# Kernel tuning notes

Measured on AMD Instinct MI355X. Metric: run time of the kernel, lower is better.

Reference implementation:

```python
import jax, jax.numpy as jnp
import numpy as np

D_MODEL = 1024
EXPAND = 2
D_INNER = D_MODEL * EXPAND
KERNEL = 4
EPS = 1e-5


def setup_inputs() -> dict:
    key = jax.random.key(0)
    ks = jax.random.split(key, 8)
    B, L = 2, 4096
    x = jax.random.normal(ks[0], (B, L, D_MODEL), dtype=jnp.float32)
    norm_w = jnp.ones((D_MODEL,), jnp.float32)
    norm_b = jnp.zeros((D_MODEL,), jnp.float32)
    # torch Linear weight layout [out, in]
    in_proj_w = jax.random.normal(ks[1], (2 * D_INNER, D_MODEL), jnp.float32) / np.sqrt(D_MODEL)
    # depthwise Conv1d weight [d_inner, 1, K]
    conv_w = jax.random.normal(ks[2], (D_INNER, 1, KERNEL), jnp.float32) / np.sqrt(KERNEL)
    conv_b = jax.random.normal(ks[3], (D_INNER,), jnp.float32) * 0.02
    gate_w = jax.random.normal(ks[4], (D_INNER, D_INNER), jnp.float32) / np.sqrt(D_INNER)
    gate_b = jnp.zeros((D_INNER,), jnp.float32)
    out_proj_w = jax.random.normal(ks[5], (D_MODEL, D_INNER), jnp.float32) / np.sqrt(D_INNER)
    return {"x": x, "norm_w": norm_w, "norm_b": norm_b, "in_proj_w": in_proj_w,
            "conv_w": conv_w, "conv_b": conv_b, "gate_w": gate_w, "gate_b": gate_b,
            "out_proj_w": out_proj_w}


def _layernorm(x, w, b):
    mu = jnp.mean(x, axis=-1, keepdims=True)
    var = jnp.var(x, axis=-1, keepdims=True)
    return (x - mu) * jax.lax.rsqrt(var + EPS) * w + b


def _glru(x, norm_w, norm_b, in_proj_w, conv_w, conv_b, gate_w, gate_b, out_proj_w):
    B, L, D = x.shape
    residual = x
    xn = _layernorm(x, norm_w, norm_b)
    xz = jnp.einsum('bld,ed->ble', xn, in_proj_w)  # [B,L,2*d_inner]
    x_inner, z = jnp.split(xz, 2, axis=-1)
    # causal depthwise conv: torch pads 3 both sides then slices [:L] == left-pad 3
    lhs = jnp.transpose(x_inner, (0, 2, 1))  # [B, C, L]
    conv = jax.lax.conv_general_dilated(
        lhs, conv_w, window_strides=(1,), padding=[(KERNEL - 1, 0)],
        feature_group_count=D_INNER,
        dimension_numbers=('NCH', 'OIH', 'NCH'))
    x_conv = jnp.transpose(conv, (0, 2, 1)) + conv_b  # [B, L, C]
    x_conv = jax.nn.silu(x_conv)
    a = jax.nn.sigmoid(jnp.einsum('blc,ec->ble', x_conv, gate_w) + gate_b)
    b = (1.0 - a) * x_conv
    # h_t = a_t * h_{t-1} + b_t, h_0 prior = 0 -> parallel associative scan
    def combine(e1, e2):
        a1, b1 = e1
        a2, b2 = e2
        return a1 * a2, a2 * b1 + b2
    _, y = jax.lax.associative_scan(combine, (a, b), axis=1)
    y = y * jax.nn.silu(z)
    return residual + jnp.einsum('blc,dc->bld', y, out_proj_w)


def reference(x, norm_w, norm_b, in_proj_w, conv_w, conv_b, gate_w, gate_b, out_proj_w):
    return _glru(x, norm_w, norm_b, in_proj_w, conv_w, conv_b, gate_w, gate_b, out_proj_w)
```

## Files before the change

kernel.cpp:

```cpp
#include <hip/hip_runtime.h>
#include <cstdint>

#define D_MODEL 1024
#define D_INNER 2048
#define LSEQ    4096
#define BATCH   2
#define M_ROWS  (BATCH * LSEQ)
#define CHUNK   128
#define NCHUNK  (LSEQ / CHUNK)

typedef unsigned short u16;
typedef __bf16 bf16x8 __attribute__((ext_vector_type(8)));
typedef float f32x4 __attribute__((ext_vector_type(4)));
typedef u16 u16x4 __attribute__((ext_vector_type(4)));

__device__ __forceinline__ u16 f2bf(float f) {
  union { float f; unsigned u; } x; x.f = f;
  unsigned u = x.u;
  unsigned r = (u + 0x7FFFu + ((u >> 16) & 1u)) >> 16;
  return (u16)r;
}
__device__ __forceinline__ float bf2f(u16 h) {
  union { unsigned u; float f; } x; x.u = ((unsigned)h) << 16;
  return x.f;
}
__device__ __forceinline__ float sigmoidf_(float v) { return 1.0f / (1.0f + expf(-v)); }
__device__ __forceinline__ float siluf_(float v)    { return v / (1.0f + expf(-v)); }

__device__ __forceinline__ void gl_lds16(const void* g, void* l) {
  __builtin_amdgcn_global_load_lds(
      (const __attribute__((address_space(1))) void*)g,
      (__attribute__((address_space(3))) void*)l, 16, 0, 0);
}

#define SBAR()   asm volatile("s_barrier" ::: "memory")
#define WAITV0() asm volatile("s_waitcnt vmcnt(0)" ::: "memory")
#define WAITV4() asm volatile("s_waitcnt vmcnt(4)" ::: "memory")

__global__ void __launch_bounds__(256)
cast_bf16_kernel(const float* __restrict__ in, u16* __restrict__ out, int n4) {
  int i = blockIdx.x * 256 + threadIdx.x;
  if (i < n4) {
    float4 v = ((const float4*)in)[i];
    u16x4 o;
    o.x = f2bf(v.x); o.y = f2bf(v.y); o.z = f2bf(v.z); o.w = f2bf(v.w);
    ((u16x4*)out)[i] = o;
  }
}

__global__ void __launch_bounds__(256)
ln_kernel(const float* __restrict__ x, const float* __restrict__ w,
          const float* __restrict__ b, u16* __restrict__ xn) {
  const int row = blockIdx.x;
  const int t = threadIdx.x;
  const float4 v = ((const float4*)(x + (size_t)row * D_MODEL))[t];
  float s  = v.x + v.y + v.z + v.w;
  float ss = v.x * v.x + v.y * v.y + v.z * v.z + v.w * v.w;
#pragma unroll
  for (int o = 32; o > 0; o >>= 1) {
    s  += __shfl_xor(s, o);
    ss += __shfl_xor(ss, o);
  }
  __shared__ float red[8];
  const int wid = t >> 6, lane = t & 63;
  if (lane == 0) { red[wid] = s; red[4 + wid] = ss; }
  __syncthreads();
  s  = red[0] + red[1] + red[2] + red[3];
  ss = red[4] + red[5] + red[6] + red[7];
  const float mu  = s * (1.0f / D_MODEL);
  const float var = ss * (1.0f / D_MODEL) - mu * mu;
  const float rs  = rsqrtf(var + 1e-5f);
  const float4 wv = ((const float4*)w)[t];
  const float4 bv = ((const float4*)b)[t];
  u16x4 o4;
  o4.x = f2bf((v.x - mu) * rs * wv.x + bv.x);
  o4.y = f2bf((v.y - mu) * rs * wv.y + bv.y);
  o4.z = f2bf((v.z - mu) * rs * wv.z + bv.z);
  o4.w = f2bf((v.w - mu) * rs * wv.w + bv.w);
  ((u16x4*)(xn + (size_t)row * D_MODEL))[t] = o4;
}

#define MFMA_BF16 __builtin_amdgcn_mfma_f32_16x16x32_bf16

template<int EPI>
__global__ void __launch_bounds__(256, 2)
gemm128(const u16* __restrict__ A, const u16* __restrict__ Bm,
        int M, int N, int K,
        const float* __restrict__ ef, float* __restrict__ of,
        u16* __restrict__ ob0, u16* __restrict__ ob1) {
  __shared__ __align__(1024) char lds[65536];
  const int tid  = threadIdx.x;
  const int wid  = tid >> 6, lane = tid & 63;
  const int nbx  = N >> 7;
  const int nwg  = nbx * (M >> 7);
  const int bid  = blockIdx.x;
  const int cpx  = nwg >> 3;
  const int swzb = (bid & 7) * cpx + (bid >> 3);
  const int bx   = swzb % nbx, by = swzb / nbx;
  const size_t m0 = (size_t)by << 7, n0 = (size_t)bx << 7;
  const int wr = wid >> 1, wc = wid & 1;
  const size_t rb = (size_t)K * 2;

  const int sslot = (((lane & 3) ^ ((lane >> 3) & 3)) << 4);
  const char* gA = (const char*)A  + (m0 + (size_t)(wid * 16 + (lane >> 2))) * rb + sslot;
  const char* gB = (const char*)Bm + (n0 + (size_t)(wid * 16 + (lane >> 2))) * rb + sslot;
  const int sd = wid * 1024;

  const int q = lane >> 4, r15 = lane & 15;
  const int xr = ((q ^ ((r15 >> 1) & 3)) << 4);
  const int aoff = (wr * 64 + r15) * 64 + xr;
  const int boff = (wc * 64 + r15) * 64 + xr;

  f32x4 acc[4][4] = {};
  const int nk = K >> 6;

  auto STG = [&](const char* g, char* ldsbase, int kk, int r0, size_t kbv) {
    gl_lds16(g + kbv + kk * 64 + (size_t)r0 * rb, ldsbase + kk * 8192 + r0 * 64 + sd);
  };

  STG(gA, lds, 0, 0, 0); STG(gA, lds, 0, 64, 0);
  STG(gB, lds + 16384, 0, 0, 0); STG(gB, lds + 16384, 0, 64, 0);
  STG(gA, lds, 1, 0, 0); STG(gA, lds, 1, 64, 0);
  STG(gB, lds + 16384, 1, 0, 0); STG(gB, lds + 16384, 1, 64, 0);
  WAITV4();
  SBAR();

  size_t kb = 128;
  for (int t = 0; t < nk; ++t) {
    const int cur = t & 1;
    const char* Ac = lds + cur * 32768;
    const char* Bc = Ac + 16384;
    char* An = lds + ((cur ^ 1) * 32768);
    char* Bn = An + 16384;
    const bool pf = (t + 1 < nk);
    bf16x8 af[4], bf[4];

    if (pf) {
      STG(gA, An, 0, 0, kb); STG(gA, An, 0, 64, kb);
      STG(gB, Bn, 0, 0, kb); STG(gB, Bn, 0, 64, kb);
    }
#pragma unroll
    for (int mi = 0; mi < 4; ++mi) af[mi] = *(const bf16x8*)(Ac + aoff + mi * 1024);
#pragma unroll
    for (int ni = 0; ni < 4; ++ni) bf[ni] = *(const bf16x8*)(Bc + boff + ni * 1024);
    __builtin_amdgcn_s_setprio(1);
#pragma unroll
    for (int mi = 0; mi < 4; ++mi)
#pragma unroll
      for (int ni = 0; ni < 4; ++ni)
        acc[mi][ni] = MFMA_BF16(af[mi], bf[ni], acc[mi][ni], 0, 0, 0);
    __builtin_amdgcn_s_setprio(0);
    if (pf) { WAITV4(); } else { WAITV0(); }
    SBAR();

    if (pf) {
      STG(gA, An, 1, 0, kb); STG(gA, An, 1, 64, kb);
      STG(gB, Bn, 1, 0, kb); STG(gB, Bn, 1, 64, kb);
    }
#pragma unroll
    for (int mi = 0; mi < 4; ++mi) af[mi] = *(const bf16x8*)(Ac + 8192 + aoff + mi * 1024);
#pragma unroll
    for (int ni = 0; ni < 4; ++ni) bf[ni] = *(const bf16x8*)(Bc + 8192 + boff + ni * 1024);
    __builtin_amdgcn_s_setprio(1);
#pragma unroll
    for (int mi = 0; mi < 4; ++mi)
#pragma unroll
      for (int ni = 0; ni < 4; ++ni)
        acc[mi][ni] = MFMA_BF16(af[mi], bf[ni], acc[mi][ni], 0, 0, 0);
    __builtin_amdgcn_s_setprio(0);
    if (pf) { WAITV4(); SBAR(); }
    kb += 128;
  }

  const int c0 = lane & 15;
  const int r0 = (lane >> 4) << 2;
  const bool isz = (EPI == 0) && (n0 >= (size_t)D_INNER);
#pragma unroll
  for (int mi = 0; mi < 4; ++mi) {
#pragma unroll
    for (int ni = 0; ni < 4; ++ni) {
#pragma unroll
      for (int rg = 0; rg < 4; ++rg) {
        const size_t row = m0 + (size_t)(wr * 64 + mi * 16 + r0 + rg);
        const size_t col = n0 + (size_t)(wc * 64 + ni * 16 + c0);
        const float v = acc[mi][ni][rg];
        if (EPI == 0) {
          if (!isz) ob0[row * D_INNER + col] = f2bf(v);
          else      ob1[row * D_INNER + (col - D_INNER)] = f2bf(siluf_(v));
        } else if (EPI == 1) {
          ob0[row * (size_t)N + col] = f2bf(v);
        } else {
          of[row * (size_t)N + col] = v + ef[row * (size_t)N + col];
        }
      }
    }
  }
}

__global__ void __launch_bounds__(256)
conv_silu_kernel(const u16* __restrict__ xin, const float* __restrict__ cw,
                 const float* __restrict__ cb, u16* __restrict__ xc) {
  const int c   = blockIdx.x * 256 + threadIdx.x;
  const int l0  = blockIdx.y * 8;
  const int bat = blockIdx.z;
  const size_t base = ((size_t)bat * LSEQ) * D_INNER + c;
  const float w0 = cw[c * 4 + 0], w1 = cw[c * 4 + 1], w2 = cw[c * 4 + 2], w3 = cw[c * 4 + 3];
  const float bb = cb[c];
  float v[11];
#pragma unroll
  for (int i = 0; i < 11; ++i) {
    const int l = l0 - 3 + i;
    v[i] = (l >= 0) ? bf2f(xin[base + (size_t)l * D_INNER]) : 0.0f;
  }
#pragma unroll
  for (int r = 0; r < 8; ++r) {
    const float acc = bb + w0 * v[r] + w1 * v[r + 1] + w2 * v[r + 2] + w3 * v[r + 3];
    xc[base + (size_t)(l0 + r) * D_INNER] = f2bf(siluf_(acc));
  }
}

__global__ void __launch_bounds__(256)
scan_a_kernel(const u16* __restrict__ g, const u16* __restrict__ xc,
              const float* __restrict__ gbias,
              float* __restrict__ cA, float* __restrict__ cB) {
  const int c   = (blockIdx.x * 256 + threadIdx.x) * 2;
  const int ch  = blockIdx.y;
  const int bat = blockIdx.z;
  const float bb0 = gbias[c], bb1 = gbias[c + 1];
  size_t idx = ((size_t)bat * LSEQ + (size_t)ch * CHUNK) * D_INNER + c;
  float pA0 = 1.0f, hB0 = 0.0f, pA1 = 1.0f, hB1 = 0.0f;
  for (int t = 0; t < CHUNK; ++t) {
    const ushort2 gg = *(const ushort2*)(g + idx);
    const ushort2 xx = *(const ushort2*)(xc + idx);
    const float a0 = sigmoidf_(bf2f(gg.x) + bb0);
    const float a1 = sigmoidf_(bf2f(gg.y) + bb1);
    pA0 *= a0; hB0 = a0 * hB0 + (1.0f - a0) * bf2f(xx.x);
    pA1 *= a1; hB1 = a1 * hB1 + (1.0f - a1) * bf2f(xx.y);
    idx += D_INNER;
  }
  const size_t o = ((size_t)bat * NCHUNK + ch) * D_INNER + c;
  *(float2*)(cA + o) = make_float2(pA0, pA1);
  *(float2*)(cB + o) = make_float2(hB0, hB1);
}

__global__ void __launch_bounds__(256)
scan_b_kernel(const float* __restrict__ cA, const float* __restrict__ cB,
              float* __restrict__ carry) {
  const int tid = blockIdx.x * 256 + threadIdx.x;
  const int bat = tid >> 11;
  const int c   = tid & (D_INNER - 1);
  float h = 0.0f;
  const size_t base = (size_t)bat * NCHUNK * D_INNER + c;
  for (int i = 0; i < NCHUNK; ++i) {
    const size_t o = base + (size_t)i * D_INNER;
    carry[o] = h;
    h = cA[o] * h + cB[o];
  }
}

__global__ void __launch_bounds__(256)
scan_c_kernel(const u16* __restrict__ g, const u16* __restrict__ xc,
              const u16* __restrict__ sz, const float* __restrict__ gbias,
              const float* __restrict__ carry, u16* __restrict__ yg) {
  const int c   = (blockIdx.x * 256 + threadIdx.x) * 2;
  const int ch  = blockIdx.y;
  const int bat = blockIdx.z;
  const float bb0 = gbias[c], bb1 = gbias[c + 1];
  const float2 h2 = *(const float2*)(carry + ((size_t)bat * NCHUNK + ch) * D_INNER + c);
  float h0 = h2.x, h1 = h2.y;
  size_t idx = ((size_t)bat * LSEQ + (size_t)ch * CHUNK) * D_INNER + c;
  for (int t = 0; t < CHUNK; ++t) {
    const ushort2 gg = *(const ushort2*)(g + idx);
    const ushort2 xx = *(const ushort2*)(xc + idx);
    const ushort2 zz = *(const ushort2*)(sz + idx);
    const float a0 = sigmoidf_(bf2f(gg.x) + bb0);
    const float a1 = sigmoidf_(bf2f(gg.y) + bb1);
    h0 = a0 * h0 + (1.0f - a0) * bf2f(xx.x);
    h1 = a1 * h1 + (1.0f - a1) * bf2f(xx.y);
    ushort2 o2;
    o2.x = f2bf(h0 * bf2f(zz.x));
    o2.y = f2bf(h1 * bf2f(zz.y));
    *(ushort2*)(yg + idx) = o2;
    idx += D_INNER;
  }
}

extern "C" void kernel_launch(void* const* d_in, const int* in_sizes, int n_in,
                              void* d_out, int out_size, void* d_ws, size_t ws_size,
                              hipStream_t stream) {
  const float* x         = (const float*)d_in[0];
  const float* norm_w    = (const float*)d_in[1];
  const float* norm_b    = (const float*)d_in[2];
  const float* in_proj_w = (const float*)d_in[3];
  const float* conv_w    = (const float*)d_in[4];
  const float* conv_b    = (const float*)d_in[5];
  const float* gate_w    = (const float*)d_in[6];
  const float* gate_b    = (const float*)d_in[7];
  const float* out_proj_w= (const float*)d_in[8];
  float* out = (float*)d_out;

  char* p = (char*)d_ws;
  u16* xn      = (u16*)p; p += (size_t)M_ROWS * D_MODEL * 2;
  u16* w_in    = (u16*)p; p += (size_t)2 * D_INNER * D_MODEL * 2;
  u16* w_gate  = (u16*)p; p += (size_t)D_INNER * D_INNER * 2;
  u16* w_out   = (u16*)p; p += (size_t)D_MODEL * D_INNER * 2;
  u16* x_inner = (u16*)p; p += (size_t)M_ROWS * D_INNER * 2;
  u16* szb     = (u16*)p; p += (size_t)M_ROWS * D_INNER * 2;
  u16* xconv   = (u16*)p; p += (size_t)M_ROWS * D_INNER * 2;
  u16* gbuf    = (u16*)p; p += (size_t)M_ROWS * D_INNER * 2;
  u16* yg      = (u16*)p; p += (size_t)M_ROWS * D_INNER * 2;
  float* cA    = (float*)p; p += (size_t)BATCH * NCHUNK * D_INNER * 4;
  float* cB    = (float*)p; p += (size_t)BATCH * NCHUNK * D_INNER * 4;
  float* carry = (float*)p; p += (size_t)BATCH * NCHUNK * D_INNER * 4;
  if ((size_t)(p - (char*)d_ws) > ws_size) return;

  cast_bf16_kernel<<<dim3(2 * D_INNER * D_MODEL / 4 / 256), 256, 0, stream>>>(in_proj_w, w_in, 2 * D_INNER * D_MODEL / 4);
  cast_bf16_kernel<<<dim3(D_INNER * D_INNER / 4 / 256), 256, 0, stream>>>(gate_w, w_gate, D_INNER * D_INNER / 4);
  cast_bf16_kernel<<<dim3(D_MODEL * D_INNER / 4 / 256), 256, 0, stream>>>(out_proj_w, w_out, D_MODEL * D_INNER / 4);

  ln_kernel<<<dim3(M_ROWS), 256, 0, stream>>>(x, norm_w, norm_b, xn);

  gemm128<0><<<dim3((M_ROWS / 128) * (2 * D_INNER / 128)), 256, 0, stream>>>(
      xn, w_in, M_ROWS, 2 * D_INNER, D_MODEL, nullptr, nullptr, x_inner, szb);

  conv_silu_kernel<<<dim3(D_INNER / 256, LSEQ / 8, BATCH), 256, 0, stream>>>(x_inner, conv_w, conv_b, xconv);

  gemm128<1><<<dim3((M_ROWS / 128) * (D_INNER / 128)), 256, 0, stream>>>(
      xconv, w_gate, M_ROWS, D_INNER, D_INNER, nullptr, nullptr, gbuf, nullptr);

  scan_a_kernel<<<dim3(D_INNER / 512, NCHUNK, BATCH), 256, 0, stream>>>(gbuf, xconv, gate_b, cA, cB);
  scan_b_kernel<<<dim3(BATCH * D_INNER / 256), 256, 0, stream>>>(cA, cB, carry);
  scan_c_kernel<<<dim3(D_INNER / 512, NCHUNK, BATCH), 256, 0, stream>>>(gbuf, xconv, szb, gate_b, carry, yg);

  gemm128<2><<<dim3((M_ROWS / 128) * (D_MODEL / 128)), 256, 0, stream>>>(
      yg, w_out, M_ROWS, D_MODEL, D_INNER, x, out, nullptr, nullptr);
}
```

Baseline: 362.9 us.

## Add 256x256 8-wave ping-pong GEMM for in_proj and gate projections

Adds a new GEMM kernel with 512 threads and 256x256 output tiles. It uses 128 KB of LDS, double-buffered with 128-wide K steps, and interleaves global-to-LDS staging with MFMA phases separated by barriers. Each wave now covers 128x64, which raises arithmetic intensity per LDS byte and cuts global traffic per FLOP. The in_proj and gate GEMMs use it; the out_proj GEMM stays on the old 128x128 kernel. In exchange there is one block per CU, fewer workgroups (256 and 128), and many barriers per iteration.

```diff
diff --git a/kernel.cpp b/kernel.cpp
--- a/kernel.cpp
+++ b/kernel.cpp
@@ -36,6 +36,7 @@
 #define SBAR()   asm volatile("s_barrier" ::: "memory")
 #define WAITV0() asm volatile("s_waitcnt vmcnt(0)" ::: "memory")
 #define WAITV4() asm volatile("s_waitcnt vmcnt(4)" ::: "memory")
+#define WAITL0() do { asm volatile("s_waitcnt lgkmcnt(0)" ::: "memory"); __builtin_amdgcn_sched_barrier(0); } while (0)
 
 __global__ void __launch_bounds__(256)
 cast_bf16_kernel(const float* __restrict__ in, u16* __restrict__ out, int n4) {
@@ -81,6 +82,157 @@
 }
 
 #define MFMA_BF16 __builtin_amdgcn_mfma_f32_16x16x32_bf16
+
+template<int EPI>
+__global__ void __launch_bounds__(512, 1)
+gemm8p(const u16* __restrict__ A, const u16* __restrict__ Bm,
+       int M, int N, int K,
+       const float* __restrict__ ef, float* __restrict__ of,
+       u16* __restrict__ ob0, u16* __restrict__ ob1) {
+  __shared__ __align__(1024) char lds[131072];
+  const int tid  = threadIdx.x;
+  const int wid  = tid >> 6, lane = tid & 63;
+  const int nbx  = N >> 8;
+  const int nwg  = nbx * (M >> 8);
+  const int bid  = blockIdx.x;
+  const int cpx  = nwg >> 3;
+  const int swzb = (bid & 7) * cpx + (bid >> 3);
+  const int bx   = swzb % nbx, by = swzb / nbx;
+  const size_t m0 = (size_t)by << 8, n0 = (size_t)bx << 8;
+  const int wr = wid >> 2, wc = wid & 3;
+  const size_t rb = (size_t)K * 2;
+
+  const int strow = lane >> 3;
+  const int stchk = (lane & 7) ^ strow;
+  const char* gA = (const char*)A  + (m0 + (size_t)(wid * 8 + strow)) * rb + stchk * 16;
+  const char* gB = (const char*)Bm + (n0 + (size_t)(wid * 8 + strow)) * rb + stchk * 16;
+  const int sdw = wid * 1024;
+
+  auto ST_A = [&](int t, int h) {
+    char* d = lds + (t & 1) * 32768 + h * 16384 + sdw;
+    const char* s = gA + (size_t)t * 128 + (size_t)(h * 128) * rb;
+    gl_lds16(s, d);
+    gl_lds16(s + 64 * rb, d + 8192);
+  };
+  auto ST_B = [&](int t, int h) {
+    char* d = lds + 65536 + (t & 1) * 32768 + h * 16384 + sdw;
+    const char* s = gB + (size_t)t * 128 + (size_t)(h * 128) * rb;
+    gl_lds16(s, d);
+    gl_lds16(s + 64 * rb, d + 8192);
+  };
+
+  const int q = lane >> 4, r15 = lane & 15;
+  const int kx0 = ((q ^ (r15 & 7)) << 4);
+  const int kx1 = (((4 + q) ^ (r15 & 7)) << 4);
+  const int arow = r15 * 128;
+  const int brow = ((wc & 1) * 64 + r15) * 128;
+  const char* aE = lds + wr * 16384;
+  const char* bE = lds + 65536 + (wc >> 1) * 16384;
+  const char* aO = aE + 32768;
+  const char* bO = bE + 32768;
+
+  bf16x8 af[8], bf[4];
+  f32x4 acc[8][4] = {};
+
+#define RD_A(kx, base)  _Pragma("unroll") \
+    for (int mf = 0; mf < 8; ++mf) af[mf] = *(const bf16x8*)((base) + mf * 2048 + arow + (kx));
+#define RD_B(kx, base)  _Pragma("unroll") \
+    for (int nf = 0; nf < 4; ++nf) bf[nf] = *(const bf16x8*)((base) + nf * 2048 + brow + (kx));
+#define MM_LO() do { __builtin_amdgcn_s_setprio(1); _Pragma("unroll") \
+    for (int mf = 0; mf < 8; ++mf) { \
+      acc[mf][0] = MFMA_BF16(af[mf], bf[0], acc[mf][0], 0, 0, 0); \
+      acc[mf][1] = MFMA_BF16(af[mf], bf[1], acc[mf][1], 0, 0, 0); } \
+    __builtin_amdgcn_s_setprio(0); } while (0)
+#define MM_HI() do { __builtin_amdgcn_s_setprio(1); _Pragma("unroll") \
+    for (int mf = 0; mf < 8; ++mf) { \
+      acc[mf][2] = MFMA_BF16(af[mf], bf[2], acc[mf][2], 0, 0, 0); \
+      acc[mf][3] = MFMA_BF16(af[mf], bf[3], acc[mf][3], 0, 0, 0); } \
+    __builtin_amdgcn_s_setprio(0); } while (0)
+
+  const int nk = K >> 6;
+  const int nIter = nk >> 1;
+
+  ST_A(0, 0); ST_A(0, 1); ST_B(0, 0); ST_B(0, 1);
+  ST_A(1, 0); ST_A(1, 1);
+  WAITV4();
+  SBAR();
+
+  for (int i = 0; i < nIter; ++i) {
+    const int t1 = 2 * i + 1, t2 = 2 * i + 2, t3 = 2 * i + 3;
+    const bool pf = (t2 < nk);
+
+    RD_A(kx0, aE); RD_B(kx0, bE);
+    ST_B(t1, 0);
+    SBAR(); WAITL0();
+    MM_LO();
+    SBAR();
+
+    ST_B(t1, 1);
+    SBAR();
+    MM_HI();
+    SBAR();
+
+    RD_A(kx1, aE); RD_B(kx1, bE);
+    SBAR(); WAITL0();
+    MM_LO();
+    SBAR();
+
+    if (pf) { ST_A(t2, 0); ST_A(t2, 1); WAITV4(); } else { WAITV0(); }
+    SBAR();
+    MM_HI();
+    SBAR();
+
+    RD_A(kx0, aO); RD_B(kx0, bO);
+    if (pf) ST_B(t2, 0);
+    SBAR(); WAITL0();
+    MM_LO();
+    SBAR();
+
+    if (pf) ST_B(t2, 1);
+    SBAR();
+    MM_HI();
+    SBAR();
+
+    RD_A(kx1, aO); RD_B(kx1, bO);
+    SBAR(); WAITL0();
+    MM_LO();
+    SBAR();
+
+    if (pf) { ST_A(t3, 0); ST_A(t3, 1); WAITV4(); }
+    SBAR();
+    MM_HI();
+    SBAR();
+  }
+
+#undef RD_A
+#undef RD_B
+#undef MM_LO
+#undef MM_HI
+
+  const int c0 = lane & 15;
+  const int r0 = (lane >> 4) << 2;
+  const bool isz = (EPI == 0) && (n0 >= (size_t)D_INNER);
+#pragma unroll
+  for (int mf = 0; mf < 8; ++mf) {
+#pragma unroll
+    for (int nf = 0; nf < 4; ++nf) {
+#pragma unroll
+      for (int rg = 0; rg < 4; ++rg) {
+        const size_t row = m0 + (size_t)(wr * 128 + mf * 16 + r0 + rg);
+        const size_t col = n0 + (size_t)(wc * 64 + nf * 16 + c0);
+        const float v = acc[mf][nf][rg];
+        if (EPI == 0) {
+          if (!isz) ob0[row * D_INNER + col] = f2bf(v);
+          else      ob1[row * D_INNER + (col - D_INNER)] = f2bf(siluf_(v));
+        } else if (EPI == 1) {
+          ob0[row * (size_t)N + col] = f2bf(v);
+        } else {
+          of[row * (size_t)N + col] = v + ef[row * (size_t)N + col];
+        }
+      }
+    }
+  }
+}
 
 template<int EPI>
 __global__ void __launch_bounds__(256, 2)
@@ -114,8 +266,8 @@
   f32x4 acc[4][4] = {};
   const int nk = K >> 6;
 
-  auto STG = [&](const char* g, char* ldsbase, int kk, int r0, size_t kbv) {
-    gl_lds16(g + kbv + kk * 64 + (size_t)r0 * rb, ldsbase + kk * 8192 + r0 * 64 + sd);
+  auto STG = [&](const char* g, char* ldsbase, int kk, int r0v, size_t kbv) {
+    gl_lds16(g + kbv + kk * 64 + (size_t)r0v * rb, ldsbase + kk * 8192 + r0v * 64 + sd);
   };
 
   STG(gA, lds, 0, 0, 0); STG(gA, lds, 0, 64, 0);
@@ -133,7 +285,7 @@
     char* An = lds + ((cur ^ 1) * 32768);
     char* Bn = An + 16384;
     const bool pf = (t + 1 < nk);
-    bf16x8 af[4], bf[4];
+    bf16x8 af[4], bfv[4];
 
     if (pf) {
       STG(gA, An, 0, 0, kb); STG(gA, An, 0, 64, kb);
@@ -142,13 +294,13 @@
 #pragma unroll
     for (int mi = 0; mi < 4; ++mi) af[mi] = *(const bf16x8*)(Ac + aoff + mi * 1024);
 #pragma unroll
-    for (int ni = 0; ni < 4; ++ni) bf[ni] = *(const bf16x8*)(Bc + boff + ni * 1024);
+    for (int ni = 0; ni < 4; ++ni) bfv[ni] = *(const bf16x8*)(Bc + boff + ni * 1024);
     __builtin_amdgcn_s_setprio(1);
 #pragma unroll
     for (int mi = 0; mi < 4; ++mi)
 #pragma unroll
       for (int ni = 0; ni < 4; ++ni)
-        acc[mi][ni] = MFMA_BF16(af[mi], bf[ni], acc[mi][ni], 0, 0, 0);
+        acc[mi][ni] = MFMA_BF16(af[mi], bfv[ni], acc[mi][ni], 0, 0, 0);
     __builtin_amdgcn_s_setprio(0);
     if (pf) { WAITV4(); } else { WAITV0(); }
     SBAR();
@@ -160,13 +312,13 @@
 #pragma unroll
     for (int mi = 0; mi < 4; ++mi) af[mi] = *(const bf16x8*)(Ac + 8192 + aoff + mi * 1024);
 #pragma unroll
-    for (int ni = 0; ni < 4; ++ni) bf[ni] = *(const bf16x8*)(Bc + 8192 + boff + ni * 1024);
+    for (int ni = 0; ni < 4; ++ni) bfv[ni] = *(const bf16x8*)(Bc + 8192 + boff + ni * 1024);
     __builtin_amdgcn_s_setprio(1);
 #pragma unroll
     for (int mi = 0; mi < 4; ++mi)
 #pragma unroll
       for (int ni = 0; ni < 4; ++ni)
-        acc[mi][ni] = MFMA_BF16(af[mi], bf[ni], acc[mi][ni], 0, 0, 0);
+        acc[mi][ni] = MFMA_BF16(af[mi], bfv[ni], acc[mi][ni], 0, 0, 0);
     __builtin_amdgcn_s_setprio(0);
     if (pf) { WAITV4(); SBAR(); }
     kb += 128;
@@ -320,12 +472,12 @@
 
   ln_kernel<<<dim3(M_ROWS), 256, 0, stream>>>(x, norm_w, norm_b, xn);
 
-  gemm128<0><<<dim3((M_ROWS / 128) * (2 * D_INNER / 128)), 256, 0, stream>>>(
+  gemm8p<0><<<dim3((M_ROWS / 256) * (2 * D_INNER / 256)), 512, 0, stream>>>(
       xn, w_in, M_ROWS, 2 * D_INNER, D_MODEL, nullptr, nullptr, x_inner, szb);
 
   conv_silu_kernel<<<dim3(D_INNER / 256, LSEQ / 8, BATCH), 256, 0, stream>>>(x_inner, conv_w, conv_b, xconv);
 
-  gemm128<1><<<dim3((M_ROWS / 128) * (D_INNER / 128)), 256, 0, stream>>>(
+  gemm8p<1><<<dim3((M_ROWS / 256) * (D_INNER / 256)), 512, 0, stream>>>(
       xconv, w_gate, M_ROWS, D_INNER, D_INNER, nullptr, nullptr, gbuf, nullptr);
 
   scan_a_kernel<<<dim3(D_INNER / 512, NCHUNK, BATCH), 256, 0, stream>>>(gbuf, xconv, gate_b, cA, cB);
```

Measured after the change: 378.2 us. 4.2% more time.

## Replace 128x128 GEMM with 256-row register-staged tile and fuse weight casts

Applied to the files above, without the earlier changes.

The GEMM now uses 512-thread workgroups with a 256xBN tile (BN 256 for the first two projections, 128 for the output projection), so each wave computes an 8xNF fragment block. Global-to-LDS copies go through registers with a new XOR swizzle instead of direct global_load_lds, and a single barrier is used per 64-wide K step. The three weight-cast launches are merged into one kernel. Larger tiles raise data reuse and arithmetic intensity. In exchange they use more registers and LDS (up to 128KB per block, which limits occupancy) and give fewer workgroups on the output GEMM.

```diff
diff --git a/kernel.cpp b/kernel.cpp
--- a/kernel.cpp
+++ b/kernel.cpp
@@ -27,25 +27,26 @@
 __device__ __forceinline__ float sigmoidf_(float v) { return 1.0f / (1.0f + expf(-v)); }
 __device__ __forceinline__ float siluf_(float v)    { return v / (1.0f + expf(-v)); }
 
-__device__ __forceinline__ void gl_lds16(const void* g, void* l) {
-  __builtin_amdgcn_global_load_lds(
-      (const __attribute__((address_space(1))) void*)g,
-      (__attribute__((address_space(3))) void*)l, 16, 0, 0);
-}
-
 #define SBAR()   asm volatile("s_barrier" ::: "memory")
-#define WAITV0() asm volatile("s_waitcnt vmcnt(0)" ::: "memory")
-#define WAITV4() asm volatile("s_waitcnt vmcnt(4)" ::: "memory")
-
-__global__ void __launch_bounds__(256)
-cast_bf16_kernel(const float* __restrict__ in, u16* __restrict__ out, int n4) {
+#define WAITL0() asm volatile("s_waitcnt lgkmcnt(0)" ::: "memory")
+
+__global__ void __launch_bounds__(256)
+cast3_kernel(const float* __restrict__ w0, const float* __restrict__ w1,
+             const float* __restrict__ w2, u16* __restrict__ o0,
+             u16* __restrict__ o1, u16* __restrict__ o2) {
+  const int n04 = 2 * D_INNER * D_MODEL / 4;
+  const int n14 = D_INNER * D_INNER / 4;
+  const int n24 = D_MODEL * D_INNER / 4;
   int i = blockIdx.x * 256 + threadIdx.x;
-  if (i < n4) {
-    float4 v = ((const float4*)in)[i];
-    u16x4 o;
-    o.x = f2bf(v.x); o.y = f2bf(v.y); o.z = f2bf(v.z); o.w = f2bf(v.w);
-    ((u16x4*)out)[i] = o;
-  }
+  const float* src; u16* dst; int j;
+  if (i < n04)            { src = w0; dst = o0; j = i; }
+  else if (i < n04 + n14) { src = w1; dst = o1; j = i - n04; }
+  else if (i < n04 + n14 + n24) { src = w2; dst = o2; j = i - n04 - n14; }
+  else return;
+  float4 v = ((const float4*)src)[j];
+  u16x4 o;
+  o.x = f2bf(v.x); o.y = f2bf(v.y); o.z = f2bf(v.z); o.w = f2bf(v.w);
+  ((u16x4*)dst)[j] = o;
 }
 
 __global__ void __launch_bounds__(256)
@@ -82,93 +83,103 @@
 
 #define MFMA_BF16 __builtin_amdgcn_mfma_f32_16x16x32_bf16
 
-template<int EPI>
-__global__ void __launch_bounds__(256, 2)
-gemm128(const u16* __restrict__ A, const u16* __restrict__ Bm,
-        int M, int N, int K,
-        const float* __restrict__ ef, float* __restrict__ of,
-        u16* __restrict__ ob0, u16* __restrict__ ob1) {
-  __shared__ __align__(1024) char lds[65536];
-  const int tid  = threadIdx.x;
-  const int wid  = tid >> 6, lane = tid & 63;
-  const int nbx  = N >> 7;
-  const int nwg  = nbx * (M >> 7);
-  const int bid  = blockIdx.x;
-  const int cpx  = nwg >> 3;
+template<int EPI, int BN>
+__global__ void __launch_bounds__(512, 2)
+gemmR(const u16* __restrict__ A, const u16* __restrict__ Bm,
+      int M, int N, int K,
+      const float* __restrict__ ef, float* __restrict__ of,
+      u16* __restrict__ ob0, u16* __restrict__ ob1) {
+  constexpr int NF  = BN / 64;
+  constexpr int NBL = BN / 64;
+  constexpr int BBY = BN * 128;
+  __shared__ __align__(1024) char lds[65536 + 2 * BBY];
+  const int tid = threadIdx.x, wid = tid >> 6, lane = tid & 63;
+  const int nbx = N / BN;
+  const int nwg = nbx * (M >> 8);
+  const int bid = blockIdx.x;
+  const int cpx = nwg >> 3;
   const int swzb = (bid & 7) * cpx + (bid >> 3);
-  const int bx   = swzb % nbx, by = swzb / nbx;
-  const size_t m0 = (size_t)by << 7, n0 = (size_t)bx << 7;
-  const int wr = wid >> 1, wc = wid & 1;
+  const int bx = swzb % nbx, by = swzb / nbx;
+  const size_t m0 = (size_t)by << 8;
+  const size_t n0 = (size_t)bx * BN;
+  const int wr = wid >> 2, wc = wid & 3;
   const size_t rb = (size_t)K * 2;
 
-  const int sslot = (((lane & 3) ^ ((lane >> 3) & 3)) << 4);
-  const char* gA = (const char*)A  + (m0 + (size_t)(wid * 16 + (lane >> 2))) * rb + sslot;
-  const char* gB = (const char*)Bm + (n0 + (size_t)(wid * 16 + (lane >> 2))) * rb + sslot;
-  const int sd = wid * 1024;
+  const int strow = lane >> 3;
+  const int stchk = (lane & 7) ^ strow;
+  const char* gA = (const char*)A  + (m0 + (size_t)(wid * 8 + strow)) * rb + stchk * 16;
+  const char* gB = (const char*)Bm + (n0 + (size_t)(wid * 8 + strow)) * rb + stchk * 16;
+  const int vb = wid * 1024 + lane * 16;
 
   const int q = lane >> 4, r15 = lane & 15;
-  const int xr = ((q ^ ((r15 >> 1) & 3)) << 4);
-  const int aoff = (wr * 64 + r15) * 64 + xr;
-  const int boff = (wc * 64 + r15) * 64 + xr;
-
-  f32x4 acc[4][4] = {};
+  const int kx0 = ((q ^ (r15 & 7)) << 4);
+  const int kx1 = (((4 + q) ^ (r15 & 7)) << 4);
+  const int arow = (wr * 128 + r15) * 128;
+  const int brow = (wc * (BN / 4) + r15) * 128;
+
+  f32x4 acc[8][NF] = {};
   const int nk = K >> 6;
-
-  auto STG = [&](const char* g, char* ldsbase, int kk, int r0, size_t kbv) {
-    gl_lds16(g + kbv + kk * 64 + (size_t)r0 * rb, ldsbase + kk * 8192 + r0 * 64 + sd);
-  };
-
-  STG(gA, lds, 0, 0, 0); STG(gA, lds, 0, 64, 0);
-  STG(gB, lds + 16384, 0, 0, 0); STG(gB, lds + 16384, 0, 64, 0);
-  STG(gA, lds, 1, 0, 0); STG(gA, lds, 1, 64, 0);
-  STG(gB, lds + 16384, 1, 0, 0); STG(gB, lds + 16384, 1, 64, 0);
-  WAITV4();
+  bf16x8 rA[4], rB[NBL];
+
+#pragma unroll
+  for (int j = 0; j < 4; ++j)   rA[j] = *(const bf16x8*)(gA + (size_t)(j * 64) * rb);
+#pragma unroll
+  for (int j = 0; j < NBL; ++j) rB[j] = *(const bf16x8*)(gB + (size_t)(j * 64) * rb);
+#pragma unroll
+  for (int j = 0; j < 4; ++j)   *(bf16x8*)(lds + j * 8192 + vb) = rA[j];
+#pragma unroll
+  for (int j = 0; j < NBL; ++j) *(bf16x8*)(lds + 65536 + j * 8192 + vb) = rB[j];
+  WAITL0();
   SBAR();
 
   size_t kb = 128;
   for (int t = 0; t < nk; ++t) {
-    const int cur = t & 1;
-    const char* Ac = lds + cur * 32768;
-    const char* Bc = Ac + 16384;
-    char* An = lds + ((cur ^ 1) * 32768);
-    char* Bn = An + 16384;
+    const int par = t & 1;
+    const char* Ac = lds + par * 32768;
+    const char* Bc = lds + 65536 + par * BBY;
+    char* An = lds + (par ^ 1) * 32768;
+    char* Bn = lds + 65536 + (par ^ 1) * BBY;
     const bool pf = (t + 1 < nk);
-    bf16x8 af[4], bf[4];
 
     if (pf) {
-      STG(gA, An, 0, 0, kb); STG(gA, An, 0, 64, kb);
-      STG(gB, Bn, 0, 0, kb); STG(gB, Bn, 0, 64, kb);
+#pragma unroll
+      for (int j = 0; j < 4; ++j)   rA[j] = *(const bf16x8*)(gA + kb + (size_t)(j * 64) * rb);
+#pragma unroll
+      for (int j = 0; j < NBL; ++j) rB[j] = *(const bf16x8*)(gB + kb + (size_t)(j * 64) * rb);
     }
-#pragma unroll
-    for (int mi = 0; mi < 4; ++mi) af[mi] = *(const bf16x8*)(Ac + aoff + mi * 1024);
-#pragma unroll
-    for (int ni = 0; ni < 4; ++ni) bf[ni] = *(const bf16x8*)(Bc + boff + ni * 1024);
+
+    bf16x8 af[8], bfv[NF];
+#pragma unroll
+    for (int mf = 0; mf < 8; ++mf) af[mf] = *(const bf16x8*)(Ac + arow + mf * 2048 + kx0);
+#pragma unroll
+    for (int nf = 0; nf < NF; ++nf) bfv[nf] = *(const bf16x8*)(Bc + brow + nf * 2048 + kx0);
     __builtin_amdgcn_s_setprio(1);
 #pragma unroll
-    for (int mi = 0; mi < 4; ++mi)
-#pragma unroll
-      for (int ni = 0; ni < 4; ++ni)
-        acc[mi][ni] = MFMA_BF16(af[mi], bf[ni], acc[mi][ni], 0, 0, 0);
+    for (int mf = 0; mf < 8; ++mf)
+#pragma unroll
+      for (int nf = 0; nf < NF; ++nf)
+        acc[mf][nf] = MFMA_BF16(af[mf], bfv[nf], acc[mf][nf], 0, 0, 0);
     __builtin_amdgcn_s_setprio(0);
-    if (pf) { WAITV4(); } else { WAITV0(); }
+#pragma unroll
+    for (int mf = 0; mf < 8; ++mf) af[mf] = *(const bf16x8*)(Ac + arow + mf * 2048 + kx1);
+#pragma unroll
+    for (int nf = 0; nf < NF; ++nf) bfv[nf] = *(const bf16x8*)(Bc + brow + nf * 2048 + kx1);
+    __builtin_amdgcn_s_setprio(1);
+#pragma unroll
+    for (int mf = 0; mf < 8; ++mf)
+#pragma unroll
+      for (int nf = 0; nf < NF; ++nf)
+        acc[mf][nf] = MFMA_BF16(af[mf], bfv[nf], acc[mf][nf], 0, 0, 0);
+    __builtin_amdgcn_s_setprio(0);
+
+    if (pf) {
+#pragma unroll
+      for (int j = 0; j < 4; ++j)   *(bf16x8*)(An + j * 8192 + vb) = rA[j];
+#pragma unroll
+      for (int j = 0; j < NBL; ++j) *(bf16x8*)(Bn + j * 8192 + vb) = rB[j];
+    }
+    WAITL0();
     SBAR();
-
-    if (pf) {
-      STG(gA, An, 1, 0, kb); STG(gA, An, 1, 64, kb);
-      STG(gB, Bn, 1, 0, kb); STG(gB, Bn, 1, 64, kb);
-    }
-#pragma unroll
-    for (int mi = 0; mi < 4; ++mi) af[mi] = *(const bf16x8*)(Ac + 8192 + aoff + mi * 1024);
-#pragma unroll
-    for (int ni = 0; ni < 4; ++ni) bf[ni] = *(const bf16x8*)(Bc + 8192 + boff + ni * 1024);
-    __builtin_amdgcn_s_setprio(1);
-#pragma unroll
-    for (int mi = 0; mi < 4; ++mi)
-#pragma unroll
-      for (int ni = 0; ni < 4; ++ni)
-        acc[mi][ni] = MFMA_BF16(af[mi], bf[ni], acc[mi][ni], 0, 0, 0);
-    __builtin_amdgcn_s_setprio(0);
-    if (pf) { WAITV4(); SBAR(); }
     kb += 128;
   }
 
@@ -176,14 +187,14 @@
   const int r0 = (lane >> 4) << 2;
   const bool isz = (EPI == 0) && (n0 >= (size_t)D_INNER);
 #pragma unroll
-  for (int mi = 0; mi < 4; ++mi) {
-#pragma unroll
-    for (int ni = 0; ni < 4; ++ni) {
+  for (int mf = 0; mf < 8; ++mf) {
+#pragma unroll
+    for (int nf = 0; nf < NF; ++nf) {
 #pragma unroll
       for (int rg = 0; rg < 4; ++rg) {
-        const size_t row = m0 + (size_t)(wr * 64 + mi * 16 + r0 + rg);
-        const size_t col = n0 + (size_t)(wc * 64 + ni * 16 + c0);
-        const float v = acc[mi][ni][rg];
+        const size_t row = m0 + (size_t)(wr * 128 + mf * 16 + r0 + rg);
+        const size_t col = n0 + (size_t)(wc * (BN / 4) + nf * 16 + c0);
+        const float v = acc[mf][nf][rg];
         if (EPI == 0) {
           if (!isz) ob0[row * D_INNER + col] = f2bf(v);
           else      ob1[row * D_INNER + (col - D_INNER)] = f2bf(siluf_(v));
@@ -314,24 +325,24 @@
   float* carry = (float*)p; p += (size_t)BATCH * NCHUNK * D_INNER * 4;
   if ((size_t)(p - (char*)d_ws) > ws_size) return;
 
-  cast_bf16_kernel<<<dim3(2 * D_INNER * D_MODEL / 4 / 256), 256, 0, stream>>>(in_proj_w, w_in, 2 * D_INNER * D_MODEL / 4);
-  cast_bf16_kernel<<<dim3(D_INNER * D_INNER / 4 / 256), 256, 0, stream>>>(gate_w, w_gate, D_INNER * D_INNER / 4);
-  cast_bf16_kernel<<<dim3(D_MODEL * D_INNER / 4 / 256), 256, 0, stream>>>(out_proj_w, w_out, D_MODEL * D_INNER / 4);
+  const int ncast4 = (2 * D_INNER * D_MODEL + D_INNER * D_INNER + D_MODEL * D_INNER) / 4;
+  cast3_kernel<<<dim3((ncast4 + 255) / 256), 256, 0, stream>>>(
+      in_proj_w, gate_w, out_proj_w, w_in, w_gate, w_out);
 
   ln_kernel<<<dim3(M_ROWS), 256, 0, stream>>>(x, norm_w, norm_b, xn);
 
-  gemm128<0><<<dim3((M_ROWS / 128) * (2 * D_INNER / 128)), 256, 0, stream>>>(
+  gemmR<0, 256><<<dim3((M_ROWS / 256) * (2 * D_INNER / 256)), 512, 0, stream>>>(
       xn, w_in, M_ROWS, 2 * D_INNER, D_MODEL, nullptr, nullptr, x_inner, szb);
 
   conv_silu_kernel<<<dim3(D_INNER / 256, LSEQ / 8, BATCH), 256, 0, stream>>>(x_inner, conv_w, conv_b, xconv);
 
-  gemm128<1><<<dim3((M_ROWS / 128) * (D_INNER / 128)), 256, 0, stream>>>(
+  gemmR<1, 256><<<dim3((M_ROWS / 256) * (D_INNER / 256)), 512, 0, stream>>>(
       xconv, w_gate, M_ROWS, D_INNER, D_INNER, nullptr, nullptr, gbuf, nullptr);
 
   scan_a_kernel<<<dim3(D_INNER / 512, NCHUNK, BATCH), 256, 0, stream>>>(gbuf, xconv, gate_b, cA, cB);
   scan_b_kernel<<<dim3(BATCH * D_INNER / 256), 256, 0, stream>>>(cA, cB, carry);
   scan_c_kernel<<<dim3(D_INNER / 512, NCHUNK, BATCH), 256, 0, stream>>>(gbuf, xconv, szb, gate_b, carry, yg);
 
-  gemm128<2><<<dim3((M_ROWS / 128) * (D_MODEL / 128)), 256, 0, stream>>>(
+  gemmR<2, 128><<<dim3((M_ROWS / 256) * (D_MODEL / 128)), 512, 0, stream>>>(
       yg, w_out, M_ROWS, D_MODEL, D_INNER, x, out, nullptr, nullptr);
 }
```

After: 341.2 us. 6.0% less time.
